# Optimization experiments

Measured on AMD Instinct MI355X. Metric: run time of the kernel, lower is better.

## Reference

```python
import jax, jax.numpy as jnp
import numpy as np

N, C, K, G, E = 65536, 256, 128, 32, 2097152
LN_EPS = 1e-5


def setup_inputs() -> dict:
    key = jax.random.key(0)
    ks = jax.random.split(key, 16)
    inp = {
        "x": jax.random.normal(ks[0], (N, C), jnp.float32),
        "evals_batch": jax.random.uniform(ks[1], (G * K,), jnp.float32),
        "evecs": jax.random.normal(ks[2], (N, K), jnp.float32),
        "mass": jax.random.uniform(ks[3], (N,), jnp.float32),
        "row": jax.random.randint(ks[4], (E,), 0, N),
        "col": jax.random.randint(ks[5], (E,), 0, N),
        "vals": jax.random.normal(ks[6], (E,), jnp.float32),
        # learned parameters (torch Linear convention: weight is [out, in])
        "t_params": jnp.full((C,), 0.5, jnp.float32),
        "grad_W": jax.random.normal(ks[7], (C, C), jnp.float32) / np.sqrt(C),
        "grad_b": jnp.zeros((C,), jnp.float32),
        "W1": jax.random.normal(ks[8], (C, 2 * C), jnp.float32) / np.sqrt(2 * C),
        "b1": jnp.zeros((C,), jnp.float32),
        "W2": jax.random.normal(ks[9], (C, C), jnp.float32) / np.sqrt(C),
        "b2": jnp.zeros((C,), jnp.float32),
        "ln_g": jnp.ones((C,), jnp.float32),
        "ln_b": jnp.zeros((C,), jnp.float32),
    }
    return inp


def reference(x, evals_batch, evecs, mass, row, col, vals,
              t_params, grad_W, grad_b, W1, b1, W2, b2, ln_g, ln_b):
    # batch is contiguous with G equal-size graphs of n nodes each
    n = N // G
    t = jnp.abs(t_params)                                   # [C]
    xg = x.reshape(G, n, C)
    eg = evecs.reshape(G, n, K)
    mg = mass.reshape(G, n)
    ev = evals_batch.reshape(G, K)
    # spectral diffusion, batched over graphs
    x_spec = jnp.einsum('gnk,gnc->gkc', eg, xg * mg[..., None])      # [G,K,C]
    decay = jnp.exp(-t[None, None, :] * jnp.clip(ev, 0.0)[..., None])  # [G,K,C]
    diff_out = jnp.einsum('gnk,gkc->gnc', eg, x_spec * decay).reshape(N, C)
    # sparse gradient operator: grad_feat = grad_X_sparse @ x  (COO)
    grad_feat = jax.ops.segment_sum(vals[:, None] * x[col], row, num_segments=N)
    grad_feat = grad_feat @ grad_W.T + grad_b
    # MLP (dropout is identity at eval)
    fused = jnp.concatenate([diff_out, grad_feat], axis=-1)           # [N,2C]
    h = jax.nn.relu(fused @ W1.T + b1)
    fused = h @ W2.T + b2
    # residual + LayerNorm
    y = x + fused
    mu = jnp.mean(y, axis=-1, keepdims=True)
    var = jnp.var(y, axis=-1, keepdims=True)
    return (y - mu) * jax.lax.rsqrt(var + LN_EPS) * ln_g + ln_b
```

## Files before the change

kernel.cpp:

```cpp
#include <hip/hip_runtime.h>

typedef unsigned short u16;
typedef unsigned long long u64;
using short8 = __attribute__((ext_vector_type(8))) short;
using f32x4  = __attribute__((ext_vector_type(4))) float;
using h16x4  = __attribute__((ext_vector_type(4))) _Float16;

constexpr int N_  = 65536;
constexpr int C_  = 256;
constexpr int K_  = 128;
constexpr int G_  = 32;
constexpr int NG_ = 2048;
constexpr int E_  = 2097152;
constexpr int NBIN_ = 2048;
constexpr int CAPB_ = 1280;
constexpr int NCHK_ = 256;

__device__ __forceinline__ u16 f2bf(float f) {
  unsigned u = __float_as_uint(f);
  unsigned r = u + 0x7FFF + ((u >> 16) & 1);
  return (u16)(r >> 16);
}
__device__ __forceinline__ float bf2f(u16 h) { return __uint_as_float((unsigned)h << 16); }
__device__ __forceinline__ u16 f2h(float f) {
  _Float16 h = (_Float16)f;
  u16 b; __builtin_memcpy(&b, &h, 2);
  return b;
}

__device__ __forceinline__ void gload_lds16(const void* g, void* l) {
  __builtin_amdgcn_global_load_lds((const __attribute__((address_space(1))) void*)g,
                                   (__attribute__((address_space(3))) void*)l, 16, 0, 0);
}

constexpr int EPI_BF16  = 0;
constexpr int EPI_DECAY = 3;
constexpr int EPI_TRANS = 4;

template <int BM, int BN, int EPI>
__device__ __forceinline__ void gemm_body(
    char* smem, int bx, int by, int z,
    const u16* __restrict__ A, long sAz, int lda,
    const u16* __restrict__ B, long sBz, int ldb,
    int Kd,
    void* __restrict__ outp, long sCz, int ldc,
    const float* __restrict__ tpar, const float* __restrict__ evptr) {
  constexpr int WM = BM / 2, WN = BN / 2;
  constexpr int FM = WM / 16, FN = WN / 16;
  u16* Asm = (u16*)smem;
  u16* Bsm = Asm + BM * 32;
  const u16* Ab = A + (long)z * sAz + (long)bx * BM * lda;
  const u16* Bb = B + (long)z * sBz + (long)by * BN * ldb;
  int tid = threadIdx.x;
  int wave = tid >> 6, lane = tid & 63;
  int wm = wave >> 1, wn = wave & 1;

  f32x4 acc[FM][FN];
  #pragma unroll
  for (int m = 0; m < FM; ++m)
    #pragma unroll
    for (int n = 0; n < FN; ++n) acc[m][n] = {0.f, 0.f, 0.f, 0.f};

  const u16* aA = Ab + (size_t)(wave * 16 + (lane >> 2)) * lda + (lane & 3) * 8;
  const u16* aB = Bb + (size_t)(wave * 16 + (lane >> 2)) * ldb + (lane & 3) * 8;
  u16* lA = Asm + wave * 512;
  u16* lB = Bsm + wave * 512;
  int arow = wm * WM + (lane & 15);
  int brow = wn * WN + (lane & 15);
  int kof = (lane >> 4) * 8;

  for (int k0 = 0; k0 < Kd; k0 += 32) {
    #pragma unroll
    for (int j = 0; j < BM / 64; ++j) gload_lds16(aA + (size_t)j * 64 * lda + k0, lA + j * 2048);
    #pragma unroll
    for (int j = 0; j < BN / 64; ++j) gload_lds16(aB + (size_t)j * 64 * ldb + k0, lB + j * 2048);
    __syncthreads();
    short8 af[FM], bfr[FN];
    #pragma unroll
    for (int m = 0; m < FM; ++m) af[m] = *(const short8*)(Asm + (arow + m * 16) * 32 + kof);
    #pragma unroll
    for (int n = 0; n < FN; ++n) bfr[n] = *(const short8*)(Bsm + (brow + n * 16) * 32 + kof);
    #pragma unroll
    for (int m = 0; m < FM; ++m)
      #pragma unroll
      for (int n = 0; n < FN; ++n)
        acc[m][n] = __builtin_amdgcn_mfma_f32_16x16x32_bf16(af[m], bfr[n], acc[m][n], 0, 0, 0);
    __syncthreads();
  }

  #pragma unroll
  for (int m = 0; m < FM; ++m) {
    #pragma unroll
    for (int n = 0; n < FN; ++n) {
      int cc = by * BN + wn * WN + n * 16 + (lane & 15);
      int rb = bx * BM + wm * WM + m * 16 + ((lane >> 4) << 2);
      if constexpr (EPI == EPI_TRANS) {
        ushort4 o = {f2bf(acc[m][n][0]), f2bf(acc[m][n][1]), f2bf(acc[m][n][2]), f2bf(acc[m][n][3])};
        *(ushort4*)((u16*)outp + (long)z * sCz + (long)cc * ldc + rb) = o;
      } else if constexpr (EPI == EPI_DECAY) {
        float tv = fabsf(tpar[cc]);
        #pragma unroll
        for (int r = 0; r < 4; ++r) {
          float ee = fmaxf(evptr[(size_t)z * K_ + rb + r], 0.f);
          ((u16*)outp)[(long)z * sCz + (long)(rb + r) * ldc + cc] = f2bf(acc[m][n][r] * __expf(-tv * ee));
        }
      } else {
        #pragma unroll
        for (int r = 0; r < 4; ++r)
          ((u16*)outp)[(long)z * sCz + (long)(rb + r) * ldc + cc] = f2bf(acc[m][n][r]);
      }
    }
  }
}

template <int BM, int BN, int EPI>
__global__ __launch_bounds__(256) void k_gemm(
    const u16* __restrict__ A, long sAz, int lda,
    const u16* __restrict__ B, long sBz, int ldb,
    int Kd,
    void* __restrict__ outp, long sCz, int ldc,
    const float* __restrict__ tpar, const float* __restrict__ evptr) {
  __shared__ __align__(16) char smem[(BM + BN) * 32 * 2];
  gemm_body<BM, BN, EPI>(smem, blockIdx.x, blockIdx.y, blockIdx.z,
                         A, sAz, lda, B, sBz, ldb, Kd, outp, sCz, ldc, tpar, evptr);
}

constexpr int PA_HIST = NCHK_;
constexpr int PA_CVX  = 4096;
constexpr int PA_CVE  = 2048;
constexpr int PA_W1   = 512;
constexpr int PA_W2   = 256;
constexpr int PA_T256 = 16;
constexpr int PA_BC   = 16;
constexpr int PA_TOTAL = PA_HIST + PA_CVX + PA_CVE + PA_W1 + PA_W2 + PA_T256 + PA_BC;

__global__ __launch_bounds__(256) void k_phaseA(
    const int* __restrict__ row, int* __restrict__ bh,
    const float* __restrict__ x, const float* __restrict__ mass,
    u16* __restrict__ xhf, u16* __restrict__ xmT,
    const float* __restrict__ evecs, u16* __restrict__ Ebf, u16* __restrict__ EbfT,
    const float* __restrict__ W1, u16* __restrict__ W1bf,
    const float* __restrict__ W2, u16* __restrict__ W2bf,
    const float* __restrict__ gW, u16* __restrict__ gWT,
    const float* __restrict__ gb, const float* __restrict__ b1, float* __restrict__ bc) {
  __shared__ __align__(16) char smem[64 * 65 * 4 + 256];
  float (*tile)[65] = (float(*)[65])smem;
  float* msm = (float*)(smem + 64 * 65 * 4);
  int id = blockIdx.x, tid = threadIdx.x;

  if (id < PA_HIST) {
    int* hist = (int*)smem;
    #pragma unroll
    for (int j = 0; j < 8; ++j) hist[tid + j * 256] = 0;
    __syncthreads();
    int e0 = id * 8192 + tid;
    #pragma unroll 4
    for (int i = 0; i < 32; ++i)
      atomicAdd(&hist[row[e0 + i * 256] >> 5], 1);
    __syncthreads();
    #pragma unroll
    for (int j = 0; j < 8; ++j) {
      int bin = tid + j * 256;
      bh[(size_t)bin * NCHK_ + id] = hist[bin];
    }
    return;
  }
  id -= PA_HIST;
  if (id < PA_CVX) {
    int r0 = (id >> 2) * 64, c0 = (id & 3) * 64;
    int tr = tid >> 4, tc4 = (tid & 15) * 4;
    #pragma unroll
    for (int p = 0; p < 4; ++p) {
      int r = p * 16 + tr;
      float4 v = *(const float4*)&x[(size_t)(r0 + r) * C_ + c0 + tc4];
      tile[r][tc4 + 0] = v.x; tile[r][tc4 + 1] = v.y; tile[r][tc4 + 2] = v.z; tile[r][tc4 + 3] = v.w;
      ushort4 o = {f2h(v.x), f2h(v.y), f2h(v.z), f2h(v.w)};
      *(ushort4*)&xhf[(size_t)(r0 + r) * C_ + c0 + tc4] = o;
    }
    if (tid < 64) msm[tid] = mass[r0 + tid];
    __syncthreads();
    int g = r0 >> 11, n0 = r0 & (NG_ - 1);
    #pragma unroll
    for (int p = 0; p < 4; ++p) {
      int cl = p * 16 + tr;
      ushort4 o;
      o.x = f2bf(tile[tc4 + 0][cl] * msm[tc4 + 0]);
      o.y = f2bf(tile[tc4 + 1][cl] * msm[tc4 + 1]);
      o.z = f2bf(tile[tc4 + 2][cl] * msm[tc4 + 2]);
      o.w = f2bf(tile[tc4 + 3][cl] * msm[tc4 + 3]);
      *(ushort4*)&xmT[((size_t)g * C_ + c0 + cl) * NG_ + n0 + tc4] = o;
    }
    return;
  }
  id -= PA_CVX;
  if (id < PA_CVE) {
    int r0 = (id >> 1) * 64, c0 = (id & 1) * 64;
    int tr = tid >> 4, tc4 = (tid & 15) * 4;
    #pragma unroll
    for (int p = 0; p < 4; ++p) {
      int r = p * 16 + tr;
      float4 v = *(const float4*)&evecs[(size_t)(r0 + r) * K_ + c0 + tc4];
      tile[r][tc4 + 0] = v.x; tile[r][tc4 + 1] = v.y; tile[r][tc4 + 2] = v.z; tile[r][tc4 + 3] = v.w;
      ushort4 o = {f2bf(v.x), f2bf(v.y), f2bf(v.z), f2bf(v.w)};
      *(ushort4*)&Ebf[(size_t)(r0 + r) * K_ + c0 + tc4] = o;
    }
    __syncthreads();
    int g = r0 >> 11, n0 = r0 & (NG_ - 1);
    #pragma unroll
    for (int p = 0; p < 4; ++p) {
      int cl = p * 16 + tr;
      ushort4 o = {f2bf(tile[tc4 + 0][cl]), f2bf(tile[tc4 + 1][cl]),
                   f2bf(tile[tc4 + 2][cl]), f2bf(tile[tc4 + 3][cl])};
      *(ushort4*)&EbfT[((size_t)g * K_ + c0 + cl) * NG_ + n0 + tc4] = o;
    }
    return;
  }
  id -= PA_CVE;
  if (id < PA_W1) { int i = id * 256 + tid; W1bf[i] = f2bf(W1[i]); return; }
  id -= PA_W1;
  if (id < PA_W2) { int i = id * 256 + tid; W2bf[i] = f2bf(W2[i]); return; }
  id -= PA_W2;
  if (id < PA_T256) {
    int r0 = (id & 3) * 64, c0 = (id >> 2) * 64;
    int tr = tid >> 4, tc4 = (tid & 15) * 4;
    #pragma unroll
    for (int p = 0; p < 4; ++p) {
      int r = p * 16 + tr;
      float4 v = *(const float4*)&gW[(size_t)(r0 + r) * 256 + c0 + tc4];
      tile[r][tc4 + 0] = v.x; tile[r][tc4 + 1] = v.y; tile[r][tc4 + 2] = v.z; tile[r][tc4 + 3] = v.w;
    }
    __syncthreads();
    #pragma unroll
    for (int p = 0; p < 4; ++p) {
      int cl = p * 16 + tr;
      ushort4 o = {f2bf(tile[tc4 + 0][cl]), f2bf(tile[tc4 + 1][cl]),
                   f2bf(tile[tc4 + 2][cl]), f2bf(tile[tc4 + 3][cl])};
      *(ushort4*)&gWT[(size_t)(c0 + cl) * 256 + r0 + tc4] = o;
    }
    return;
  }
  id -= PA_T256;
  {
    float* red = (float*)smem;
    int cl = tid >> 4, js = tid & 15;
    int c = id * 16 + cl;
    const float* wrow = &W1[(size_t)c * 512 + 256 + js * 16];
    float s = 0.f;
    #pragma unroll
    for (int jj = 0; jj < 16; ++jj) s += wrow[jj] * gb[js * 16 + jj];
    red[cl * 17 + js] = s;
    __syncthreads();
    if (js == 0) {
      float tot = b1[c];
      #pragma unroll
      for (int q = 0; q < 16; ++q) tot += red[cl * 17 + q];
      bc[c] = tot;
    }
  }
}

__global__ __launch_bounds__(256) void k_scanOS(const int* __restrict__ bh, int* __restrict__ baseL,
                                                int* __restrict__ gcnt) {
  __shared__ int sc[256];
  int bin = blockIdx.x, tid = threadIdx.x;
  int v = bh[(size_t)bin * NCHK_ + tid];
  sc[tid] = v;
  __syncthreads();
  for (int o = 1; o < 256; o <<= 1) {
    int t = (tid >= o) ? sc[tid - o] : 0;
    __syncthreads();
    sc[tid] += t;
    __syncthreads();
  }
  baseL[(size_t)tid * NBIN_ + bin] = sc[tid] - v;
  if (tid == 255) gcnt[bin] = sc[255];
}

constexpr int PB_SCAT = NCHK_;
constexpr int PB_WC   = 4;
constexpr int PB_SP1  = 128;
constexpr int PB_TOTAL = PB_SCAT + PB_WC + PB_SP1;

__global__ __launch_bounds__(256) void k_phaseB(
    const int* __restrict__ row, const int* __restrict__ col, const float* __restrict__ vals,
    const int* __restrict__ baseL, u64* __restrict__ epB,
    const u16* __restrict__ W1bf, const u16* __restrict__ gWT, u16* __restrict__ Wc,
    const u16* __restrict__ EbfT, const u16* __restrict__ xmT, u16* __restrict__ S,
    const float* __restrict__ tpar, const float* __restrict__ evptr) {
  __shared__ __align__(16) char smem[16384];
  int id = blockIdx.x, tid = threadIdx.x;

  if (id < PB_SCAT) {
    int* sbase = (int*)smem;
    int* cur   = sbase + NBIN_;
    #pragma unroll
    for (int j = 0; j < 8; ++j) {
      int b = tid + j * 256;
      sbase[b] = baseL[(size_t)id * NBIN_ + b];
      cur[b] = 0;
    }
    __syncthreads();
    int e0 = id * 8192 + tid;
    #pragma unroll 4
    for (int i = 0; i < 32; ++i) {
      int e = e0 + i * 256;
      int rr = row[e];
      int b = rr >> 5;
      int rk = atomicAdd(&cur[b], 1);
      int lpos = sbase[b] + rk;
      if (lpos < CAPB_)
        epB[(size_t)b * CAPB_ + lpos] =
            ((u64)(rr & 31) << 32) | ((u64)f2h(vals[e]) << 16) | (u64)(unsigned)col[e];
    }
    return;
  }
  id -= PB_SCAT;
  if (id < PB_WC) {
    gemm_body<128, 128, EPI_BF16>(smem, id & 1, id >> 1, 0,
                                  W1bf + 256, 0, 512, gWT, 0, 256, 256,
                                  Wc, 0, 256, nullptr, nullptr);
    return;
  }
  id -= PB_WC;
  {
    int zz = id >> 2, rem = id & 3;
    gemm_body<64, 128, EPI_DECAY>(smem, rem & 1, rem >> 1, zz,
                                  EbfT, (long)K_ * NG_, NG_, xmT, (long)C_ * NG_, NG_, NG_,
                                  S, (long)K_ * C_, C_, tpar, evptr);
  }
}

__global__ __launch_bounds__(256) void k_gatherF(const u16* __restrict__ xhf, const int* __restrict__ gcnt,
                                                 const u64* __restrict__ epB, u16* __restrict__ gf) {
  __shared__ unsigned eL[CAPB_];
  __shared__ int chist[256];
  __shared__ int roff[257];
  __shared__ int sc[256];
  int b = blockIdx.x, tid = threadIdx.x;
  int wave = tid >> 6, lane = tid & 63;
  int n = gcnt[b]; if (n > CAPB_) n = CAPB_;
  chist[tid] = 0;
  __syncthreads();
  const u64* ebase = epB + (size_t)b * CAPB_;
  unsigned pkr[5]; int cellr[5]; int rkr[5];
  #pragma unroll
  for (int q = 0; q < 5; ++q) {
    int i = tid + q * 256;
    bool ok = i < n;
    u64 pk = ok ? ebase[i] : 0;
    int cell = (int)((pk & 0xFFFFu) >> 13) * 32 + ((int)(pk >> 32) & 31);
    pkr[q] = (unsigned)pk; cellr[q] = cell; rkr[q] = 0;
    if (ok) rkr[q] = atomicAdd(&chist[cell], 1);
  }
  __syncthreads();
  int s = chist[tid];
  sc[tid] = s;
  __syncthreads();
  for (int o = 1; o < 256; o <<= 1) {
    int v = (tid >= o) ? sc[tid - o] : 0;
    __syncthreads();
    sc[tid] += v;
    __syncthreads();
  }
  roff[tid] = sc[tid] - s;
  if (tid == 255) roff[256] = sc[255];
  __syncthreads();
  #pragma unroll
  for (int q = 0; q < 5; ++q) {
    int i = tid + q * 256;
    if (i < n) eL[roff[cellr[q]] + rkr[q]] = pkr[q];
  }
  __syncthreads();

  const u16* xb = xhf + lane * 4;
  f32x4 acc[8];
  #pragma unroll
  for (int k = 0; k < 8; ++k) acc[k] = {0.f, 0.f, 0.f, 0.f};
  for (int t = 0; t < 8; ++t) {
    #pragma unroll
    for (int k = 0; k < 8; ++k) {
      int cell = t * 32 + wave * 8 + k;
      int j = roff[cell], en = roff[cell + 1];
      while (j < en) {
        unsigned u[4]; h16x4 xv[4];
        #pragma unroll
        for (int q = 0; q < 4; ++q) u[q] = (j + q < en) ? eL[j + q] : 0u;
        #pragma unroll
        for (int q = 0; q < 4; ++q) xv[q] = *(const h16x4*)(xb + (size_t)(u[q] & 0xFFFFu) * C_);
        #pragma unroll
        for (int q = 0; q < 4; ++q) {
          u16 hb = (u16)(u[q] >> 16);
          _Float16 hv; __builtin_memcpy(&hv, &hb, 2);
          float v = (float)hv;
          acc[k][0] += (float)xv[q][0] * v;
          acc[k][1] += (float)xv[q][1] * v;
          acc[k][2] += (float)xv[q][2] * v;
          acc[k][3] += (float)xv[q][3] * v;
        }
        j += 4;
      }
    }
    __syncthreads();
  }
  int r0 = b * 32 + wave * 8;
  #pragma unroll
  for (int k = 0; k < 8; ++k) {
    ushort4 o = {f2bf(acc[k][0]), f2bf(acc[k][1]), f2bf(acc[k][2]), f2bf(acc[k][3])};
    *(ushort4*)&gf[(size_t)(r0 + k) * C_ + lane * 4] = o;
  }
}

__global__ __launch_bounds__(256) void k_gemm_h2(
    const u16* __restrict__ Eb, const u16* __restrict__ Tt,
    const u16* __restrict__ gf, const u16* __restrict__ Wc,
    const float* __restrict__ bc, u16* __restrict__ h) {
  __shared__ __align__(16) u16 Asm[128 * 32];
  __shared__ __align__(16) u16 Bsm[128 * 32];
  int i0 = blockIdx.x * 128;
  int g = i0 >> 11;
  int tid = threadIdx.x, wave = tid >> 6, lane = tid & 63;
  int wm = wave >> 1, wn = wave & 1;
  f32x4 acc[4][4];
  #pragma unroll
  for (int m = 0; m < 4; ++m)
    #pragma unroll
    for (int n = 0; n < 4; ++n) acc[m][n] = {0.f, 0.f, 0.f, 0.f};
  int srow = wave * 16 + (lane >> 2), scol = (lane & 3) * 8;
  u16* lA = Asm + wave * 512;
  u16* lB = Bsm + wave * 512;
  int arow = wm * 64 + (lane & 15);
  int brow = wn * 64 + (lane & 15);
  int kof = (lane >> 4) * 8;

  {
    const u16* aA = Eb + (size_t)(i0 + srow) * K_ + scol;
    const u16* aB = Tt + (size_t)g * C_ * K_ + (size_t)(blockIdx.y * 128 + srow) * K_ + scol;
    for (int k0 = 0; k0 < 128; k0 += 32) {
      gload_lds16(aA + k0, lA); gload_lds16(aA + (size_t)64 * K_ + k0, lA + 2048);
      gload_lds16(aB + k0, lB); gload_lds16(aB + (size_t)64 * K_ + k0, lB + 2048);
      __syncthreads();
      short8 af[4], bfr[4];
      #pragma unroll
      for (int m = 0; m < 4; ++m) af[m] = *(const short8*)(Asm + (arow + m * 16) * 32 + kof);
      #pragma unroll
      for (int n = 0; n < 4; ++n) bfr[n] = *(const short8*)(Bsm + (brow + n * 16) * 32 + kof);
      #pragma unroll
      for (int m = 0; m < 4; ++m)
        #pragma unroll
        for (int n = 0; n < 4; ++n)
          acc[m][n] = __builtin_amdgcn_mfma_f32_16x16x32_bf16(af[m], bfr[n], acc[m][n], 0, 0, 0);
      __syncthreads();
    }
  }
  {
    const u16* aA = gf + (size_t)(i0 + srow) * C_ + scol;
    const u16* aB = Wc + (size_t)(blockIdx.y * 128 + srow) * C_ + scol;
    for (int k0 = 0; k0 < 256; k0 += 32) {
      gload_lds16(aA + k0, lA); gload_lds16(aA + (size_t)64 * C_ + k0, lA + 2048);
      gload_lds16(aB + k0, lB); gload_lds16(aB + (size_t)64 * C_ + k0, lB + 2048);
      __syncthreads();
      short8 af[4], bfr[4];
      #pragma unroll
      for (int m = 0; m < 4; ++m) af[m] = *(const short8*)(Asm + (arow + m * 16) * 32 + kof);
      #pragma unroll
      for (int n = 0; n < 4; ++n) bfr[n] = *(const short8*)(Bsm + (brow + n * 16) * 32 + kof);
      #pragma unroll
      for (int m = 0; m < 4; ++m)
        #pragma unroll
        for (int n = 0; n < 4; ++n)
          acc[m][n] = __builtin_amdgcn_mfma_f32_16x16x32_bf16(af[m], bfr[n], acc[m][n], 0, 0, 0);
      __syncthreads();
    }
  }
  #pragma unroll
  for (int m = 0; m < 4; ++m) {
    #pragma unroll
    for (int n = 0; n < 4; ++n) {
      int cc = blockIdx.y * 128 + wn * 64 + n * 16 + (lane & 15);
      int rb = i0 + wm * 64 + m * 16 + ((lane >> 4) << 2);
      float bv = bc[cc];
      #pragma unroll
      for (int r = 0; r < 4; ++r)
        h[(size_t)(rb + r) * C_ + cc] = f2bf(fmaxf(acc[m][n][r] + bv, 0.f));
    }
  }
}

__global__ __launch_bounds__(512) void k_out(
    const u16* __restrict__ h, const u16* __restrict__ W2bf, const float* __restrict__ b2,
    const float* __restrict__ x, const float* __restrict__ lng, const float* __restrict__ lnb,
    float* __restrict__ out) {
  __shared__ __align__(16) u16 Asm[128 * 32];
  __shared__ __align__(16) u16 Bsm[256 * 32];
  __shared__ float ps1[128][4], ps2[128][4];
  int i0 = blockIdx.x * 128;
  int tid = threadIdx.x, wave = tid >> 6, lane = tid & 63;
  int wm = wave >> 2, wn = wave & 3;

  f32x4 acc[4][4];
  #pragma unroll
  for (int m = 0; m < 4; ++m)
    #pragma unroll
    for (int n = 0; n < 4; ++n) acc[m][n] = {0.f, 0.f, 0.f, 0.f};

  const u16* aA = h + (size_t)(i0 + (tid >> 2)) * C_ + (tid & 3) * 8;
  const u16* aB = W2bf + (size_t)(tid >> 2) * C_ + (tid & 3) * 8;
  u16* lA = Asm + wave * 512;
  u16* lB = Bsm + wave * 512;
  int arow = wm * 64 + (lane & 15);
  int brow = wn * 64 + (lane & 15);
  int kof = (lane >> 4) * 8;

  for (int k0 = 0; k0 < 256; k0 += 32) {
    gload_lds16(aA + k0, lA);
    gload_lds16(aB + k0, lB);
    gload_lds16(aB + (size_t)128 * C_ + k0, lB + 4096);
    __syncthreads();
    short8 af[4], bfr[4];
    #pragma unroll
    for (int m = 0; m < 4; ++m) af[m] = *(const short8*)(Asm + (arow + m * 16) * 32 + kof);
    #pragma unroll
    for (int n = 0; n < 4; ++n) bfr[n] = *(const short8*)(Bsm + (brow + n * 16) * 32 + kof);
    #pragma unroll
    for (int m = 0; m < 4; ++m)
      #pragma unroll
      for (int n = 0; n < 4; ++n)
        acc[m][n] = __builtin_amdgcn_mfma_f32_16x16x32_bf16(af[m], bfr[n], acc[m][n], 0, 0, 0);
    __syncthreads();
  }

  float bb[4], lg[4], lb[4];
  #pragma unroll
  for (int n = 0; n < 4; ++n) {
    int cc = wn * 64 + n * 16 + (lane & 15);
    bb[n] = b2[cc]; lg[n] = lng[cc]; lb[n] = lnb[cc];
  }
  #pragma unroll
  for (int m = 0; m < 4; ++m) {
    #pragma unroll
    for (int r = 0; r < 4; ++r) {
      int rl = wm * 64 + m * 16 + ((lane >> 4) << 2) + r;
      #pragma unroll
      for (int n = 0; n < 4; ++n) {
        int cc = wn * 64 + n * 16 + (lane & 15);
        acc[m][n][r] += bb[n] + x[(size_t)(i0 + rl) * C_ + cc];
      }
    }
  }
  #pragma unroll
  for (int m = 0; m < 4; ++m) {
    #pragma unroll
    for (int r = 0; r < 4; ++r) {
      float t1 = acc[m][0][r] + acc[m][1][r] + acc[m][2][r] + acc[m][3][r];
      float t2 = acc[m][0][r] * acc[m][0][r] + acc[m][1][r] * acc[m][1][r] +
                 acc[m][2][r] * acc[m][2][r] + acc[m][3][r] * acc[m][3][r];
      #pragma unroll
      for (int msk = 1; msk < 16; msk <<= 1) {
        t1 += __shfl_xor(t1, msk);
        t2 += __shfl_xor(t2, msk);
      }
      if ((lane & 15) == 0) {
        int rl = wm * 64 + m * 16 + ((lane >> 4) << 2) + r;
        ps1[rl][wn] = t1; ps2[rl][wn] = t2;
      }
    }
  }
  __syncthreads();
  #pragma unroll
  for (int m = 0; m < 4; ++m) {
    #pragma unroll
    for (int r = 0; r < 4; ++r) {
      int rl = wm * 64 + m * 16 + ((lane >> 4) << 2) + r;
      float tot1 = ps1[rl][0] + ps1[rl][1] + ps1[rl][2] + ps1[rl][3];
      float tot2 = ps2[rl][0] + ps2[rl][1] + ps2[rl][2] + ps2[rl][3];
      float mu = tot1 * (1.f / 256.f);
      float var = fmaxf(tot2 * (1.f / 256.f) - mu * mu, 0.f);
      float rs = rsqrtf(var + 1e-5f);
      #pragma unroll
      for (int n = 0; n < 4; ++n) {
        int cc = wn * 64 + n * 16 + (lane & 15);
        out[(size_t)(i0 + rl) * C_ + cc] = (acc[m][n][r] - mu) * rs * lg[n] + lb[n];
      }
    }
  }
}

extern "C" void kernel_launch(void* const* d_in, const int* in_sizes, int n_in,
                              void* d_out, int out_size, void* d_ws, size_t ws_size,
                              hipStream_t stream) {
  const float* x        = (const float*)d_in[0];
  const float* ev       = (const float*)d_in[1];
  const float* evecs    = (const float*)d_in[2];
  const float* mass     = (const float*)d_in[3];
  const int*   row      = (const int*)d_in[4];
  const int*   col      = (const int*)d_in[5];
  const float* vals     = (const float*)d_in[6];
  const float* t_params = (const float*)d_in[7];
  const float* gW       = (const float*)d_in[8];
  const float* gb       = (const float*)d_in[9];
  const float* W1       = (const float*)d_in[10];
  const float* b1       = (const float*)d_in[11];
  const float* W2       = (const float*)d_in[12];
  const float* b2       = (const float*)d_in[13];
  const float* lng      = (const float*)d_in[14];
  const float* lnb      = (const float*)d_in[15];
  float* out = (float*)d_out;

  char* p = (char*)d_ws;
  u16* xhf  = (u16*)p; p += (size_t)N_ * C_ * 2;
  u16* xmT  = (u16*)p; p += (size_t)G_ * C_ * NG_ * 2;
  u16* EbfT = (u16*)p; p += (size_t)G_ * K_ * NG_ * 2;
  u16* Ebf  = (u16*)p; p += (size_t)N_ * K_ * 2;
  u16* S    = (u16*)p; p += (size_t)G_ * K_ * C_ * 2;
  u16* Tt   = (u16*)p; p += (size_t)G_ * C_ * K_ * 2;
  u16* h    = (u16*)p; p += (size_t)N_ * C_ * 2;
  u16* W1bf = (u16*)p; p += (size_t)C_ * 512 * 2;
  u16* W2bf = (u16*)p; p += (size_t)C_ * C_ * 2;
  u16* gWT  = (u16*)p; p += (size_t)C_ * C_ * 2;
  u16* Wc   = (u16*)p; p += (size_t)C_ * C_ * 2;
  float* bc = (float*)p; p += (size_t)C_ * 4;
  int* gcnt = (int*)p; p += (size_t)NBIN_ * 4;
  int* bh   = (int*)p; p += (size_t)NBIN_ * NCHK_ * 4;
  int* baseL= (int*)p; p += (size_t)NCHK_ * NBIN_ * 4;
  u64* epB  = (u64*)p; p += (size_t)NBIN_ * CAPB_ * 8;
  u16* gf   = xmT;

  k_phaseA<<<PA_TOTAL, 256, 0, stream>>>(row, bh, x, mass, xhf, xmT,
                                         evecs, Ebf, EbfT, W1, W1bf, W2, W2bf,
                                         gW, gWT, gb, b1, bc);
  k_scanOS<<<NBIN_, 256, 0, stream>>>(bh, baseL, gcnt);
  k_phaseB<<<PB_TOTAL, 256, 0, stream>>>(row, col, vals, baseL, epB,
                                         W1bf, gWT, Wc, EbfT, xmT, S, t_params, ev);
  k_gemm<128, 128, EPI_TRANS><<<dim3(1, 2, G_), 256, 0, stream>>>(
      S, (long)K_ * C_, C_, W1bf, 0, 512, 256,
      Tt, (long)C_ * K_, K_, nullptr, nullptr);

  k_gatherF<<<NBIN_, 256, 0, stream>>>(xhf, gcnt, epB, gf);

  k_gemm_h2<<<dim3(N_ / 128, 2), 256, 0, stream>>>(Ebf, Tt, gf, Wc, bc, h);

  k_out<<<N_ / 128, 512, 0, stream>>>(h, W2bf, b2, x, lng, lnb, out);
}
```

Baseline: 343.4 us.

## Move spectral projection GEMM into merged kernel with sparse gather

Moves the decay-weighted spectral projection GEMM blocks out of the scatter kernel into a new combined kernel that also runs the per-bin sparse gather. The scatter kernel now handles only COO scattering plus the small combined-weight GEMM. The gather output gets its own workspace buffer instead of aliasing xmT, since xmT is still being read by the concurrently running GEMM blocks. This is meant to overlap the compute-bound GEMM with the memory-bound gather and balance the scatter kernel. The cost is an extra workspace buffer and shared memory sized for the larger of the two roles.

```diff
diff --git a/kernel.cpp b/kernel.cpp
--- a/kernel.cpp
+++ b/kernel.cpp
@@ -278,15 +278,12 @@
 
 constexpr int PB_SCAT = NCHK_;
 constexpr int PB_WC   = 4;
-constexpr int PB_SP1  = 128;
-constexpr int PB_TOTAL = PB_SCAT + PB_WC + PB_SP1;
+constexpr int PB_TOTAL = PB_SCAT + PB_WC;
 
 __global__ __launch_bounds__(256) void k_phaseB(
     const int* __restrict__ row, const int* __restrict__ col, const float* __restrict__ vals,
     const int* __restrict__ baseL, u64* __restrict__ epB,
-    const u16* __restrict__ W1bf, const u16* __restrict__ gWT, u16* __restrict__ Wc,
-    const u16* __restrict__ EbfT, const u16* __restrict__ xmT, u16* __restrict__ S,
-    const float* __restrict__ tpar, const float* __restrict__ evptr) {
+    const u16* __restrict__ W1bf, const u16* __restrict__ gWT, u16* __restrict__ Wc) {
   __shared__ __align__(16) char smem[16384];
   int id = blockIdx.x, tid = threadIdx.x;
 
@@ -315,28 +312,34 @@
     return;
   }
   id -= PB_SCAT;
-  if (id < PB_WC) {
-    gemm_body<128, 128, EPI_BF16>(smem, id & 1, id >> 1, 0,
-                                  W1bf + 256, 0, 512, gWT, 0, 256, 256,
-                                  Wc, 0, 256, nullptr, nullptr);
-    return;
-  }
-  id -= PB_WC;
-  {
+  gemm_body<128, 128, EPI_BF16>(smem, id & 1, id >> 1, 0,
+                                W1bf + 256, 0, 512, gWT, 0, 256, 256,
+                                Wc, 0, 256, nullptr, nullptr);
+}
+
+constexpr int PC_SP1 = 128;
+constexpr int PC_TOTAL = PC_SP1 + NBIN_;
+
+__global__ __launch_bounds__(256) void k_phaseC(
+    const u16* __restrict__ xhf, const int* __restrict__ gcnt,
+    const u64* __restrict__ epB, u16* __restrict__ gf,
+    const u16* __restrict__ EbfT, const u16* __restrict__ xmT, u16* __restrict__ S,
+    const float* __restrict__ tpar, const float* __restrict__ evptr) {
+  __shared__ __align__(16) char smem[12544];
+  int id = blockIdx.x, tid = threadIdx.x;
+
+  if (id < PC_SP1) {
     int zz = id >> 2, rem = id & 3;
     gemm_body<64, 128, EPI_DECAY>(smem, rem & 1, rem >> 1, zz,
                                   EbfT, (long)K_ * NG_, NG_, xmT, (long)C_ * NG_, NG_, NG_,
                                   S, (long)K_ * C_, C_, tpar, evptr);
-  }
-}
-
-__global__ __launch_bounds__(256) void k_gatherF(const u16* __restrict__ xhf, const int* __restrict__ gcnt,
-                                                 const u64* __restrict__ epB, u16* __restrict__ gf) {
-  __shared__ unsigned eL[CAPB_];
-  __shared__ int chist[256];
-  __shared__ int roff[257];
-  __shared__ int sc[256];
-  int b = blockIdx.x, tid = threadIdx.x;
+    return;
+  }
+  int b = id - PC_SP1;
+  unsigned* eL = (unsigned*)smem;
+  int* chist = (int*)(smem + 5120);
+  int* roff  = chist + 256;
+  int* sc    = roff + 257;
   int wave = tid >> 6, lane = tid & 63;
   int n = gcnt[b]; if (n > CAPB_) n = CAPB_;
   chist[tid] = 0;
@@ -614,6 +617,7 @@
   u16* S    = (u16*)p; p += (size_t)G_ * K_ * C_ * 2;
   u16* Tt   = (u16*)p; p += (size_t)G_ * C_ * K_ * 2;
   u16* h    = (u16*)p; p += (size_t)N_ * C_ * 2;
+  u16* gf   = (u16*)p; p += (size_t)N_ * C_ * 2;
   u16* W1bf = (u16*)p; p += (size_t)C_ * 512 * 2;
   u16* W2bf = (u16*)p; p += (size_t)C_ * C_ * 2;
   u16* gWT  = (u16*)p; p += (size_t)C_ * C_ * 2;
@@ -623,20 +627,17 @@
   int* bh   = (int*)p; p += (size_t)NBIN_ * NCHK_ * 4;
   int* baseL= (int*)p; p += (size_t)NCHK_ * NBIN_ * 4;
   u64* epB  = (u64*)p; p += (size_t)NBIN_ * CAPB_ * 8;
-  u16* gf   = xmT;
 
   k_phaseA<<<PA_TOTAL, 256, 0, stream>>>(row, bh, x, mass, xhf, xmT,
                                          evecs, Ebf, EbfT, W1, W1bf, W2, W2bf,
                                          gW, gWT, gb, b1, bc);
   k_scanOS<<<NBIN_, 256, 0, stream>>>(bh, baseL, gcnt);
-  k_phaseB<<<PB_TOTAL, 256, 0, stream>>>(row, col, vals, baseL, epB,
-                                         W1bf, gWT, Wc, EbfT, xmT, S, t_params, ev);
+  k_phaseB<<<PB_TOTAL, 256, 0, stream>>>(row, col, vals, baseL, epB, W1bf, gWT, Wc);
+  k_phaseC<<<PC_TOTAL, 256, 0, stream>>>(xhf, gcnt, epB, gf, EbfT, xmT, S, t_params, ev);
   k_gemm<128, 128, EPI_TRANS><<<dim3(1, 2, G_), 256, 0, stream>>>(
       S, (long)K_ * C_, C_, W1bf, 0, 512, 256,
       Tt, (long)C_ * K_, K_, nullptr, nullptr);
 
-  k_gatherF<<<NBIN_, 256, 0, stream>>>(xhf, gcnt, epB, gf);
-
   k_gemm_h2<<<dim3(N_ / 128, 2), 256, 0, stream>>>(Ebf, Tt, gf, Wc, bc, h);
 
   k_out<<<N_ / 128, 512, 0, stream>>>(h, W2bf, b2, x, lng, lnb, out);
```

New measurement: 359.4 us. 1.05x slower.

## Fuse first MLP GEMM with second GEMM and LayerNorm via LDS-resident hidden tile

Applied to the files above, without the earlier changes.

Merges k_gemm_h2 and k_out into one kernel, k_mlp. Each block computes a 64-row by 256-column hidden tile, applies bias and ReLU, and keeps the bf16 result in swizzled shared memory. It then runs the W2 GEMM and the residual LayerNorm from that tile, so the hidden activation is never written to or read back from global memory and one launch is removed. In exchange, tiles shrink to 64 rows, each block reloads the full Tt, Wc and W2 weights, and LDS use rises to about 50KB, which may reduce occupancy.

```diff
diff --git a/kernel.cpp b/kernel.cpp
--- a/kernel.cpp
+++ b/kernel.cpp
@@ -410,34 +410,41 @@
   }
 }
 
-__global__ __launch_bounds__(256) void k_gemm_h2(
+__global__ __launch_bounds__(256) void k_mlp(
     const u16* __restrict__ Eb, const u16* __restrict__ Tt,
     const u16* __restrict__ gf, const u16* __restrict__ Wc,
-    const float* __restrict__ bc, u16* __restrict__ h) {
-  __shared__ __align__(16) u16 Asm[128 * 32];
-  __shared__ __align__(16) u16 Bsm[128 * 32];
-  int i0 = blockIdx.x * 128;
+    const float* __restrict__ bc,
+    const u16* __restrict__ W2bf, const float* __restrict__ b2,
+    const float* __restrict__ x, const float* __restrict__ lng, const float* __restrict__ lnb,
+    float* __restrict__ out) {
+  __shared__ __align__(16) u16 Asm[64 * 32];
+  __shared__ __align__(16) u16 Bsm[256 * 32];
+  __shared__ __align__(16) u16 hs[64 * 256];
+  __shared__ float ps1[64][4], ps2[64][4];
+  int i0 = blockIdx.x * 64;
   int g = i0 >> 11;
   int tid = threadIdx.x, wave = tid >> 6, lane = tid & 63;
-  int wm = wave >> 1, wn = wave & 1;
-  f32x4 acc[4][4];
-  #pragma unroll
-  for (int m = 0; m < 4; ++m)
-    #pragma unroll
-    for (int n = 0; n < 4; ++n) acc[m][n] = {0.f, 0.f, 0.f, 0.f};
+  int wn = wave;
   int srow = wave * 16 + (lane >> 2), scol = (lane & 3) * 8;
   u16* lA = Asm + wave * 512;
   u16* lB = Bsm + wave * 512;
-  int arow = wm * 64 + (lane & 15);
+  int arow = lane & 15;
   int brow = wn * 64 + (lane & 15);
   int kof = (lane >> 4) * 8;
 
+  f32x4 acc[4][4];
+  #pragma unroll
+  for (int m = 0; m < 4; ++m)
+    #pragma unroll
+    for (int n = 0; n < 4; ++n) acc[m][n] = {0.f, 0.f, 0.f, 0.f};
+
   {
     const u16* aA = Eb + (size_t)(i0 + srow) * K_ + scol;
-    const u16* aB = Tt + (size_t)g * C_ * K_ + (size_t)(blockIdx.y * 128 + srow) * K_ + scol;
+    const u16* aB = Tt + (size_t)g * C_ * K_ + (size_t)srow * K_ + scol;
     for (int k0 = 0; k0 < 128; k0 += 32) {
-      gload_lds16(aA + k0, lA); gload_lds16(aA + (size_t)64 * K_ + k0, lA + 2048);
-      gload_lds16(aB + k0, lB); gload_lds16(aB + (size_t)64 * K_ + k0, lB + 2048);
+      gload_lds16(aA + k0, lA);
+      #pragma unroll
+      for (int j = 0; j < 4; ++j) gload_lds16(aB + (size_t)j * 64 * K_ + k0, lB + j * 2048);
       __syncthreads();
       short8 af[4], bfr[4];
       #pragma unroll
@@ -454,10 +461,11 @@
   }
   {
     const u16* aA = gf + (size_t)(i0 + srow) * C_ + scol;
-    const u16* aB = Wc + (size_t)(blockIdx.y * 128 + srow) * C_ + scol;
+    const u16* aB = Wc + (size_t)srow * C_ + scol;
     for (int k0 = 0; k0 < 256; k0 += 32) {
-      gload_lds16(aA + k0, lA); gload_lds16(aA + (size_t)64 * C_ + k0, lA + 2048);
-      gload_lds16(aB + k0, lB); gload_lds16(aB + (size_t)64 * C_ + k0, lB + 2048);
+      gload_lds16(aA + k0, lA);
+      #pragma unroll
+      for (int j = 0; j < 4; ++j) gload_lds16(aB + (size_t)j * 64 * C_ + k0, lB + j * 2048);
       __syncthreads();
       short8 af[4], bfr[4];
       #pragma unroll
@@ -473,62 +481,46 @@
     }
   }
   #pragma unroll
-  for (int m = 0; m < 4; ++m) {
-    #pragma unroll
-    for (int n = 0; n < 4; ++n) {
-      int cc = blockIdx.y * 128 + wn * 64 + n * 16 + (lane & 15);
-      int rb = i0 + wm * 64 + m * 16 + ((lane >> 4) << 2);
-      float bv = bc[cc];
-      #pragma unroll
-      for (int r = 0; r < 4; ++r)
-        h[(size_t)(rb + r) * C_ + cc] = f2bf(fmaxf(acc[m][n][r] + bv, 0.f));
-    }
-  }
-}
-
-__global__ __launch_bounds__(512) void k_out(
-    const u16* __restrict__ h, const u16* __restrict__ W2bf, const float* __restrict__ b2,
-    const float* __restrict__ x, const float* __restrict__ lng, const float* __restrict__ lnb,
-    float* __restrict__ out) {
-  __shared__ __align__(16) u16 Asm[128 * 32];
-  __shared__ __align__(16) u16 Bsm[256 * 32];
-  __shared__ float ps1[128][4], ps2[128][4];
-  int i0 = blockIdx.x * 128;
-  int tid = threadIdx.x, wave = tid >> 6, lane = tid & 63;
-  int wm = wave >> 2, wn = wave & 3;
-
-  f32x4 acc[4][4];
+  for (int n = 0; n < 4; ++n) {
+    int cc = wn * 64 + n * 16 + (lane & 15);
+    float bv = bc[cc];
+    #pragma unroll
+    for (int m = 0; m < 4; ++m) {
+      #pragma unroll
+      for (int r = 0; r < 4; ++r) {
+        int rb = m * 16 + ((lane >> 4) << 2) + r;
+        hs[(rb * 256 + cc) ^ ((rb & 7) << 3)] = f2bf(fmaxf(acc[m][n][r] + bv, 0.f));
+      }
+    }
+  }
+  __syncthreads();
+
   #pragma unroll
   for (int m = 0; m < 4; ++m)
     #pragma unroll
     for (int n = 0; n < 4; ++n) acc[m][n] = {0.f, 0.f, 0.f, 0.f};
-
-  const u16* aA = h + (size_t)(i0 + (tid >> 2)) * C_ + (tid & 3) * 8;
-  const u16* aB = W2bf + (size_t)(tid >> 2) * C_ + (tid & 3) * 8;
-  u16* lA = Asm + wave * 512;
-  u16* lB = Bsm + wave * 512;
-  int arow = wm * 64 + (lane & 15);
-  int brow = wn * 64 + (lane & 15);
-  int kof = (lane >> 4) * 8;
-
-  for (int k0 = 0; k0 < 256; k0 += 32) {
-    gload_lds16(aA + k0, lA);
-    gload_lds16(aB + k0, lB);
-    gload_lds16(aB + (size_t)128 * C_ + k0, lB + 4096);
-    __syncthreads();
-    short8 af[4], bfr[4];
-    #pragma unroll
-    for (int m = 0; m < 4; ++m) af[m] = *(const short8*)(Asm + (arow + m * 16) * 32 + kof);
-    #pragma unroll
-    for (int n = 0; n < 4; ++n) bfr[n] = *(const short8*)(Bsm + (brow + n * 16) * 32 + kof);
-    #pragma unroll
-    for (int m = 0; m < 4; ++m)
-      #pragma unroll
-      for (int n = 0; n < 4; ++n)
-        acc[m][n] = __builtin_amdgcn_mfma_f32_16x16x32_bf16(af[m], bfr[n], acc[m][n], 0, 0, 0);
-    __syncthreads();
-  }
-
+  {
+    const u16* aB = W2bf + (size_t)srow * C_ + scol;
+    for (int k0 = 0; k0 < 256; k0 += 32) {
+      #pragma unroll
+      for (int j = 0; j < 4; ++j) gload_lds16(aB + (size_t)j * 64 * C_ + k0, lB + j * 2048);
+      __syncthreads();
+      short8 af[4], bfr[4];
+      #pragma unroll
+      for (int m = 0; m < 4; ++m) {
+        int ar = arow + m * 16;
+        af[m] = *(const short8*)(hs + ((ar * 256 + k0 + kof) ^ ((ar & 7) << 3)));
+      }
+      #pragma unroll
+      for (int n = 0; n < 4; ++n) bfr[n] = *(const short8*)(Bsm + (brow + n * 16) * 32 + kof);
+      #pragma unroll
+      for (int m = 0; m < 4; ++m)
+        #pragma unroll
+        for (int n = 0; n < 4; ++n)
+          acc[m][n] = __builtin_amdgcn_mfma_f32_16x16x32_bf16(af[m], bfr[n], acc[m][n], 0, 0, 0);
+      __syncthreads();
+    }
+  }
   float bb[4], lg[4], lb[4];
   #pragma unroll
   for (int n = 0; n < 4; ++n) {
@@ -539,7 +531,7 @@
   for (int m = 0; m < 4; ++m) {
     #pragma unroll
     for (int r = 0; r < 4; ++r) {
-      int rl = wm * 64 + m * 16 + ((lane >> 4) << 2) + r;
+      int rl = m * 16 + ((lane >> 4) << 2) + r;
       #pragma unroll
       for (int n = 0; n < 4; ++n) {
         int cc = wn * 64 + n * 16 + (lane & 15);
@@ -560,7 +552,7 @@
         t2 += __shfl_xor(t2, msk);
       }
       if ((lane & 15) == 0) {
-        int rl = wm * 64 + m * 16 + ((lane >> 4) << 2) + r;
+        int rl = m * 16 + ((lane >> 4) << 2) + r;
         ps1[rl][wn] = t1; ps2[rl][wn] = t2;
       }
     }
@@ -570,7 +562,7 @@
   for (int m = 0; m < 4; ++m) {
     #pragma unroll
     for (int r = 0; r < 4; ++r) {
-      int rl = wm * 64 + m * 16 + ((lane >> 4) << 2) + r;
+      int rl = m * 16 + ((lane >> 4) << 2) + r;
       float tot1 = ps1[rl][0] + ps1[rl][1] + ps1[rl][2] + ps1[rl][3];
       float tot2 = ps2[rl][0] + ps2[rl][1] + ps2[rl][2] + ps2[rl][3];
       float mu = tot1 * (1.f / 256.f);
@@ -613,7 +605,6 @@
   u16* Ebf  = (u16*)p; p += (size_t)N_ * K_ * 2;
   u16* S    = (u16*)p; p += (size_t)G_ * K_ * C_ * 2;
   u16* Tt   = (u16*)p; p += (size_t)G_ * C_ * K_ * 2;
-  u16* h    = (u16*)p; p += (size_t)N_ * C_ * 2;
   u16* W1bf = (u16*)p; p += (size_t)C_ * 512 * 2;
   u16* W2bf = (u16*)p; p += (size_t)C_ * C_ * 2;
   u16* gWT  = (u16*)p; p += (size_t)C_ * C_ * 2;
@@ -637,7 +628,5 @@
 
   k_gatherF<<<NBIN_, 256, 0, stream>>>(xhf, gcnt, epB, gf);
 
-  k_gemm_h2<<<dim3(N_ / 128, 2), 256, 0, stream>>>(Ebf, Tt, gf, Wc, bc, h);
-
-  k_out<<<N_ / 128, 512, 0, stream>>>(h, W2bf, b2, x, lng, lnb, out);
-}
+  k_mlp<<<N_ / 64, 256, 0, stream>>>(Ebf, Tt, gf, Wc, bc, W2bf, b2, x, lng, lnb, out);
+}
```

Result: faster. 323.4 us (-5.8%).
